# Performance work log

Hardware: AMD Instinct MI355X
Metric: run time of the kernel (lower is better)

Reference implementation:

```python
import jax, jax.numpy as jnp
import numpy as np

BS, T, N = 16, 48, 147
IN = 2 * N      # input_size = 294; lstm1 hidden = input_size
H = 128         # hidden_size
AH = 8          # transformer attention heads
GH = 4          # GAT heads
OUT = 294       # output_size
DFF = 2048      # TransformerEncoderLayer default dim_feedforward
NEG = -9e15

def _u(k, shape, fan):
    return jax.random.uniform(k, shape, jnp.float32, -1.0, 1.0) / np.sqrt(fan)

def setup_inputs():
    ks = iter(jax.random.split(jax.random.key(0), 40))
    p = {}
    p['X'] = jax.random.normal(next(ks), (BS, T, IN), jnp.float32)
    p['adj_matrix'] = jax.random.randint(next(ks), (N, N), 0, 2, jnp.int32)
    p['W_trans'] = _u(next(ks), (H, IN), IN); p['b_trans'] = jnp.zeros((H,), jnp.float32)
    p['enc_in_w'] = _u(next(ks), (3 * H, H), H); p['enc_in_b'] = jnp.zeros((3 * H,), jnp.float32)
    p['enc_out_w'] = _u(next(ks), (H, H), H); p['enc_out_b'] = jnp.zeros((H,), jnp.float32)
    p['ln1_g'] = jnp.ones((H,), jnp.float32); p['ln1_b'] = jnp.zeros((H,), jnp.float32)
    p['ln2_g'] = jnp.ones((H,), jnp.float32); p['ln2_b'] = jnp.zeros((H,), jnp.float32)
    p['ff1_w'] = _u(next(ks), (DFF, H), H); p['ff1_b'] = jnp.zeros((DFF,), jnp.float32)
    p['ff2_w'] = _u(next(ks), (H, DFF), DFF); p['ff2_b'] = jnp.zeros((H,), jnp.float32)
    p['Wih1'] = _u(next(ks), (4 * IN, H), H); p['Whh1'] = _u(next(ks), (4 * IN, IN), IN)
    p['bih1'] = jnp.zeros((4 * IN,), jnp.float32); p['bhh1'] = jnp.zeros((4 * IN,), jnp.float32)
    p['gat_W1'] = _u(next(ks), (GH, 2, H), 2); p['gat_a1'] = _u(next(ks), (GH, 2 * H), 2 * H)
    p['gat_W2'] = _u(next(ks), (GH * H, H), GH * H); p['gat_a2'] = _u(next(ks), (2 * H,), 2 * H)
    p['W_sc'] = _u(next(ks), (H, 2), 2); p['b_sc'] = jnp.zeros((H,), jnp.float32)
    p['Wih2'] = _u(next(ks), (4 * H, H * N), H * N); p['Whh2'] = _u(next(ks), (4 * H, H), H)
    p['bih2'] = jnp.zeros((4 * H,), jnp.float32); p['bhh2'] = jnp.zeros((4 * H,), jnp.float32)
    p['W_fc'] = _u(next(ks), (OUT, H), H); p['b_fc'] = jnp.zeros((OUT,), jnp.float32)
    return p

def _ln(x, g, b, eps=1e-5):
    m = x.mean(-1, keepdims=True)
    v = ((x - m) ** 2).mean(-1, keepdims=True)
    return (x - m) * jax.lax.rsqrt(v + eps) * g + b

def _mha(x, in_w, in_b, out_w, out_b):
    B, S, D = x.shape
    dh = D // AH
    q, k, v = jnp.split(x @ in_w.T + in_b, 3, axis=-1)
    def rh(t):
        return t.reshape(B, S, AH, dh).transpose(0, 2, 1, 3)
    q, k, v = rh(q), rh(k), rh(v)
    att = jax.nn.softmax(jnp.einsum('bhqd,bhkd->bhqk', q, k) / np.sqrt(dh), axis=-1)
    o = jnp.einsum('bhqk,bhkd->bhqd', att, v).transpose(0, 2, 1, 3).reshape(B, S, D)
    return o @ out_w.T + out_b

def _lstm(x, Wih, Whh, bih, bhh, hid):
    B = x.shape[0]
    def step(carry, xt):
        h, c = carry
        g = xt @ Wih.T + h @ Whh.T + (bih + bhh)
        i, f, gg, o = jnp.split(g, 4, axis=-1)
        c = jax.nn.sigmoid(f) * c + jax.nn.sigmoid(i) * jnp.tanh(gg)
        h = jax.nn.sigmoid(o) * jnp.tanh(c)
        return (h, c), h
    h0 = jnp.zeros((B, hid), x.dtype)
    (hT, _), ys = jax.lax.scan(step, (h0, h0), x.transpose(1, 0, 2))
    return ys.transpose(1, 0, 2), hT

def _gat(x, adj, W1, a1, W2, a2, alpha=0.1):
    # x: [B, N, 2]; batched over all bs*num_steps graph instances; eval mode (dropout off)
    mask = (adj > 0)[None, ...]
    # layer 1: GH heads, ELU + concat
    Wh = jnp.einsum('bnf,kfh->bknh', x, W1)                        # [B,GH,N,H]
    f1 = jnp.einsum('bknh,kh->bkn', Wh, a1[:, :H])
    f2 = jnp.einsum('bknh,kh->bkn', Wh, a1[:, H:])
    e = jax.nn.leaky_relu(f1[..., :, None] + f2[..., None, :], alpha)
    att = jax.nn.softmax(jnp.where(mask[:, None], e, NEG), axis=-1)
    h1 = jax.nn.elu(jnp.einsum('bkij,bkjh->bkih', att, Wh))        # [B,GH,N,H]
    h1 = h1.transpose(0, 2, 1, 3).reshape(x.shape[0], N, GH * H)   # concat heads
    # layer 2: single output head, final ELU
    Who = h1 @ W2                                                   # [B,N,H]
    g1 = Who @ a2[:H]
    g2 = Who @ a2[H:]
    e2 = jax.nn.leaky_relu(g1[..., :, None] + g2[..., None, :], alpha)
    att2 = jax.nn.softmax(jnp.where(mask, e2, NEG), axis=-1)
    return jax.nn.elu(jnp.einsum('bij,bjh->bih', att2, Who))        # [B,N,H]

def reference(X, adj_matrix, W_trans, b_trans, enc_in_w, enc_in_b, enc_out_w, enc_out_b,
              ln1_g, ln1_b, ln2_g, ln2_b, ff1_w, ff1_b, ff2_w, ff2_b,
              Wih1, Whh1, bih1, bhh1, gat_W1, gat_a1, gat_W2, gat_a2,
              W_sc, b_sc, Wih2, Whh2, bih2, bhh2, W_fc, b_fc):
    Y = jax.nn.elu(X @ W_trans.T + b_trans)                        # [BS,T,H]
    # TransformerEncoderLayer (post-norm, ReLU FFN, eval)
    Y = _ln(Y + _mha(Y, enc_in_w, enc_in_b, enc_out_w, enc_out_b), ln1_g, ln1_b)
    Y = _ln(Y + (jax.nn.relu(Y @ ff1_w.T + ff1_b) @ ff2_w.T + ff2_b), ln2_g, ln2_b)
    Y, _ = _lstm(Y, Wih1, Whh1, bih1, bhh1, IN)                    # [BS,T,2N]
    Yg = Y.reshape(N, BS * T, 2).transpose(1, 0, 2)                # raw reshape as in torch, -> [BS*T,N,2]
    out = _gat(Yg, adj_matrix, gat_W1, gat_a1, gat_W2, gat_a2)     # [BS*T,N,H]
    out = out.transpose(1, 0, 2).reshape(BS, T, N * H)             # stack(dim=1) then reshape
    sc = jax.nn.elu(X.reshape(BS, T, N, 2) @ W_sc.T + b_sc).reshape(BS, T, N * H)
    _, hT = _lstm(out + sc, Wih2, Whh2, bih2, bhh2, H)
    return hT @ W_fc.T + b_fc                                      # [BS,OUT]
```

## Files before the change

kernel.cpp:

```cpp
#include <hip/hip_runtime.h>
#include <math.h>


typedef _Float16 half8 __attribute__((ext_vector_type(8)));
typedef _Float16 half4 __attribute__((ext_vector_type(4)));
typedef _Float16 half2v __attribute__((ext_vector_type(2)));
typedef float f32x4 __attribute__((ext_vector_type(4)));

#if __has_builtin(__builtin_amdgcn_fdot2)
#define DOT2(a,b,c) __builtin_amdgcn_fdot2((a),(b),(c),false)
#else
#define DOT2(a,b,c) ((c) + (float)(a)[0]*(float)(b)[0] + (float)(a)[1]*(float)(b)[1])
#endif

static constexpr size_t Y0o   = 0;
static constexpr size_t QKVo  = 98304;
static constexpr size_t ATTOo = 393216;
static constexpr size_t Y1o   = 491520;
static constexpr size_t Y1Ho  = 589824;
static constexpr size_t FFHo  = 638976;
static constexpr size_t PREo  = 1425408;
static constexpr size_t Y2Ho  = 1523712;
static constexpr size_t XW1o  = 1572864;
static constexpr size_t Y3o   = 2476032;
static constexpr size_t Zo    = 0;
static constexpr size_t So    = 7225344;
static constexpr size_t WHOTo = 8354304;
static constexpr size_t WFo   = 16218624;
static constexpr size_t ZGPo  = 21035520;
static constexpr size_t ZGo   = 25754112;
static constexpr size_t HTo   = 26147328;
static constexpr size_t C12o  = 26149376;
static constexpr size_t WT1Ho = 26149392;
static constexpr size_t WT2Ho = 26323440;
static constexpr size_t FF1Ho = 26356208;
static constexpr size_t FF2Ho = 26487280;
static constexpr size_t WIH1Ho= 26618352;
static constexpr size_t W2To  = 26696176;
static constexpr size_t EINTo = 26728944;
static constexpr size_t EOUTTo= 26778096;
static constexpr size_t WTRTo = 26794480;
static constexpr size_t MASKo = 26832112;
static constexpr size_t HXo   = 26833008;

__device__ __forceinline__ float eluf(float x){ return x > 0.f ? x : __expf(x)-1.f; }
__device__ __forceinline__ float sigf(float x){ return 1.f/(1.f+__expf(-x)); }

__global__ void k_prep(const float* Whh1, const float* Whh2, const float* ff1w,
                       const float* ff2w, const float* Wih1, const float* einw,
                       const float* eoutw, const float* wtr, const float* gw2, float* ws) {
  int id = blockIdx.x * 256 + threadIdx.x;
  if (id < 348096) {
    int e=id&7, r=id>>3; int row=r%168; int q=r/168; int kg=q%37; int p=q/37;
    int k=kg*8+e; int gate=row/42, jr=row-gate*42; int j=gate*294+p*42+jr;
    ((_Float16*)(ws+WT1Ho))[id] = (_Float16)((k<294)? Whh1[j*294+k] : 0.f); return; }
  id -= 348096;
  if (id < 65536) {
    int e=id&7, r=id>>3; int j=r&511, gi=r>>9; int k=gi*8+e;
    ((_Float16*)(ws+WT2Ho))[id] = (_Float16)Whh2[j*128+k]; return; }
  id -= 65536;
  if (id < 262144) { ((_Float16*)(ws+FF1Ho))[id] = (_Float16)ff1w[id]; return; }
  id -= 262144;
  if (id < 262144) { ((_Float16*)(ws+FF2Ho))[id] = (_Float16)ff2w[id]; return; }
  id -= 262144;
  if (id < 155648) { int j=id>>7, k=id&127;
    ((_Float16*)(ws+WIH1Ho))[id] = (_Float16)((j<1176)? Wih1[j*128+k] : 0.f); return; }
  id -= 155648;
  if (id < 65536)  { int h=id>>9, q=id&511;
    ((_Float16*)(ws+W2To))[id] = (_Float16)gw2[q*128+h]; return; }
  id -= 65536;
  if (id < 49152)  { int k=id/384,  j=id-k*384;  ws[EINTo+id] = einw[j*128+k]; return; }
  id -= 49152;
  if (id < 16384)  { int k=id/128,  j=id-k*128;  ws[EOUTTo+id]= eoutw[j*128+k]; return; }
  id -= 16384;
  if (id < 37632)  { int k=id/128,  j=id-k*128;  ws[WTRTo+id] = wtr[j*294+k]; return; }
}

__global__ void k_c12_mask(const float* gw1, const float* ga1, const int* adj, float* ws) {
  int tid = threadIdx.x;
  if (tid < 8) {
    int k = tid>>1, c = tid&1;
    float a=0.f, b=0.f;
    for (int h=0; h<128; ++h) {
      float w = gw1[(k*2+c)*128+h];
      a += w * ga1[k*256+h];
      b += w * ga1[k*256+128+h];
    }
    ws[C12o+tid] = a; ws[C12o+8+tid] = b;
  }
  unsigned long long* msk = (unsigned long long*)(ws + MASKo);
  for (int i = tid; i < 441; i += 256) {
    int r = i/3, w = i-r*3;
    unsigned long long b = 0ull;
    for (int bit=0; bit<64; ++bit) {
      int j = w*64+bit;
      if (j < 147 && adj[r*147+j] > 0) b |= (1ull<<bit);
    }
    msk[i] = b;
  }
  unsigned* hx = (unsigned*)(ws + HXo);
  for (int i=tid;i<9408;i+=256) hx[i]=0u;
}

__global__ void k1_trans(const float* X, const float* btr, float* ws) {
  int row = blockIdx.x, tid = threadIdx.x;
  __shared__ float xr[294];
  for (int i=tid; i<294; i+=128) xr[i] = X[row*294+i];
  __syncthreads();
  float acc = btr[tid];
  const float* w = ws + WTRTo;
  for (int k=0;k<294;++k) acc += xr[k]*w[k*128+tid];
  ws[Y0o + (size_t)row*128 + tid] = eluf(acc);
}

__global__ void k2_qkv(const float* einb, float* ws) {
  int row = blockIdx.x, tid = threadIdx.x;
  __shared__ float yr[128];
  if (tid<128) yr[tid] = ws[Y0o+(size_t)row*128+tid];
  __syncthreads();
  float acc = einb[tid];
  const float* w = ws + EINTo;
  for (int k=0;k<128;++k) acc += yr[k]*w[k*384+tid];
  ws[QKVo + (size_t)row*384 + tid] = acc;
}

__global__ void k3_attn(float* ws) {
  int bid = blockIdx.x; int bs = bid>>3, a = bid&7; int tid = threadIdx.x;
  __shared__ float q[48][16], kk[48][16], v[48][16], sc[48][49];
  for (int idx=tid; idx<768; idx+=256) {
    int t = idx>>4, d = idx&15;
    const float* base = ws + QKVo + (size_t)(bs*48+t)*384 + a*16 + d;
    q[t][d] = base[0]; kk[t][d] = base[128]; v[t][d] = base[256];
  }
  __syncthreads();
  for (int idx=tid; idx<2304; idx+=256) {
    int i = idx/48, j = idx-i*48;
    float s = 0.f;
    for (int d=0;d<16;++d) s += q[i][d]*kk[j][d];
    sc[i][j] = s*0.25f;
  }
  __syncthreads();
  if (tid < 48) {
    float mx = -INFINITY;
    for (int j=0;j<48;++j) mx = fmaxf(mx, sc[tid][j]);
    float s = 0.f;
    for (int j=0;j<48;++j){ float p = __expf(sc[tid][j]-mx); sc[tid][j]=p; s+=p; }
    float inv = 1.f/s;
    for (int j=0;j<48;++j) sc[tid][j]*=inv;
  }
  __syncthreads();
  for (int idx=tid; idx<768; idx+=256) {
    int t = idx>>4, d = idx&15;
    float s=0.f;
    for (int j=0;j<48;++j) s += sc[t][j]*v[j][d];
    ws[ATTOo + (size_t)(bs*48+t)*128 + a*16 + d] = s;
  }
}

__global__ void k4_ln1(const float* eoutb, const float* g, const float* b, float* ws) {
  int row = blockIdx.x, tid = threadIdx.x;
  __shared__ float orow[128];
  __shared__ float red[128];
  __shared__ float mv[2];
  orow[tid] = ws[ATTOo+(size_t)row*128+tid];
  __syncthreads();
  float acc = eoutb[tid] + ws[Y0o+(size_t)row*128+tid];
  const float* w = ws + EOUTTo;
  for (int k=0;k<128;++k) acc += orow[k]*w[k*128+tid];
  red[tid]=acc; __syncthreads();
  for (int s=64;s>0;s>>=1){ if(tid<s) red[tid]+=red[tid+s]; __syncthreads(); }
  if (tid==0) mv[0]=red[0]*(1.f/128.f);
  __syncthreads();
  float d = acc - mv[0];
  red[tid]=d*d; __syncthreads();
  for (int s=64;s>0;s>>=1){ if(tid<s) red[tid]+=red[tid+s]; __syncthreads(); }
  if (tid==0) mv[1]=red[0]*(1.f/128.f);
  __syncthreads();
  float val = d*rsqrtf(mv[1]+1e-5f)*g[tid]+b[tid];
  ws[Y1o+(size_t)row*128+tid] = val;
  ((_Float16*)(ws+Y1Ho))[(size_t)row*128+tid] = (_Float16)val;
}

__global__ void __launch_bounds__(256) k5g(const float* b1, float* ws) {
  int tid=threadIdx.x; int gw=blockIdx.x*4+(tid>>6);
  int l=tid&63, lr=l&15, kg=l>>4;
  int mt=gw>>5, nt=gw&31;
  const _Float16* A=(const _Float16*)(ws+Y1Ho);
  const _Float16* B=(const _Float16*)(ws+FF1Ho);
  _Float16* C=(_Float16*)(ws+FFHo);
  size_t r0=(size_t)mt*64, c0=(size_t)nt*64;
  f32x4 acc[4][4];
  #pragma unroll
  for(int a=0;a<4;++a)
    #pragma unroll
    for(int b=0;b<4;++b) acc[a][b]=(f32x4){0.f,0.f,0.f,0.f};
  #pragma unroll
  for (int s=0;s<4;++s){
    int kb=s*32+kg*8;
    half8 av[4], bv[4];
    #pragma unroll
    for(int f=0;f<4;++f) av[f]=*(const half8*)(A+(r0+f*16+lr)*128+kb);
    #pragma unroll
    for(int f=0;f<4;++f) bv[f]=*(const half8*)(B+(c0+f*16+lr)*128+kb);
    #pragma unroll
    for(int fr=0;fr<4;++fr)
      #pragma unroll
      for(int fc=0;fc<4;++fc)
        acc[fr][fc]=__builtin_amdgcn_mfma_f32_16x16x32_f16(av[fr],bv[fc],acc[fr][fc],0,0,0);
  }
  #pragma unroll
  for(int fr=0;fr<4;++fr)
    #pragma unroll
    for(int fc=0;fc<4;++fc){
      size_t col=c0+fc*16+lr;
      float bb=b1[col];
      #pragma unroll
      for(int r=0;r<4;++r){
        float v=acc[fr][fc][r]+bb; v=fmaxf(v,0.f);
        C[(r0+fr*16+kg*4+r)*2048+col]=(_Float16)v;
      }
    }
}

__global__ void __launch_bounds__(256) k6g(float* ws) {
  int tid=threadIdx.x; int gw=blockIdx.x*4+(tid>>6);
  int l=tid&63, lr=l&15, kg=l>>4;
  int ksp=gw&3, nt=(gw>>2)&1, mt=gw>>3;
  const _Float16* A=(const _Float16*)(ws+FFHo);
  const _Float16* B=(const _Float16*)(ws+FF2Ho);
  float* C=ws+ZGPo+(size_t)ksp*98304;
  size_t r0=(size_t)mt*64, c0=(size_t)nt*64;
  f32x4 acc[4][4];
  #pragma unroll
  for(int a=0;a<4;++a)
    #pragma unroll
    for(int b=0;b<4;++b) acc[a][b]=(f32x4){0.f,0.f,0.f,0.f};
  #pragma unroll
  for (int s=0;s<16;++s){
    int kb=ksp*512+s*32+kg*8;
    half8 av[4], bv[4];
    #pragma unroll
    for(int f=0;f<4;++f) av[f]=*(const half8*)(A+(r0+f*16+lr)*2048+kb);
    #pragma unroll
    for(int f=0;f<4;++f) bv[f]=*(const half8*)(B+(c0+f*16+lr)*2048+kb);
    #pragma unroll
    for(int fr=0;fr<4;++fr)
      #pragma unroll
      for(int fc=0;fc<4;++fc)
        acc[fr][fc]=__builtin_amdgcn_mfma_f32_16x16x32_f16(av[fr],bv[fc],acc[fr][fc],0,0,0);
  }
  #pragma unroll
  for(int fr=0;fr<4;++fr)
    #pragma unroll
    for(int fc=0;fc<4;++fc){
      size_t col=c0+fc*16+lr;
      #pragma unroll
      for(int r=0;r<4;++r)
        C[(r0+fr*16+kg*4+r)*128+col]=acc[fr][fc][r];
    }
}

__global__ void k6b_ln2(const float* b2, const float* g, const float* b, float* ws) {
  int row=blockIdx.x, tid=threadIdx.x;
  __shared__ float red[128];
  __shared__ float mv[2];
  float acc = ws[Y1o+(size_t)row*128+tid] + b2[tid];
  #pragma unroll
  for (int ksp=0;ksp<4;++ksp) acc += ws[ZGPo+(size_t)ksp*98304+(size_t)row*128+tid];
  red[tid]=acc; __syncthreads();
  for (int s=64;s>0;s>>=1){ if(tid<s) red[tid]+=red[tid+s]; __syncthreads(); }
  if (tid==0) mv[0]=red[0]*(1.f/128.f);
  __syncthreads();
  float d = acc - mv[0];
  red[tid]=d*d; __syncthreads();
  for (int s=64;s>0;s>>=1){ if(tid<s) red[tid]+=red[tid+s]; __syncthreads(); }
  if (tid==0) mv[1]=red[0]*(1.f/128.f);
  __syncthreads();
  float val = d*rsqrtf(mv[1]+1e-5f)*g[tid]+b[tid];
  ((_Float16*)(ws+Y2Ho))[(size_t)row*128+tid] = (_Float16)val;
}

__global__ void __launch_bounds__(256) k7g(const float* bih1, const float* bhh1, float* ws) {
  int tid=threadIdx.x; int gw=blockIdx.x*4+(tid>>6);
  int l=tid&63, lr=l&15, kg=l>>4;
  int mt=gw/19, nt=gw-mt*19;
  const _Float16* A=(const _Float16*)(ws+Y2Ho);
  const _Float16* B=(const _Float16*)(ws+WIH1Ho);
  float* C=ws+XW1o;
  size_t r0=(size_t)mt*64, c0=(size_t)nt*64;
  f32x4 acc[4][4];
  #pragma unroll
  for(int a=0;a<4;++a)
    #pragma unroll
    for(int b=0;b<4;++b) acc[a][b]=(f32x4){0.f,0.f,0.f,0.f};
  #pragma unroll
  for (int s=0;s<4;++s){
    int kb=s*32+kg*8;
    half8 av[4], bv[4];
    #pragma unroll
    for(int f=0;f<4;++f) av[f]=*(const half8*)(A+(r0+f*16+lr)*128+kb);
    #pragma unroll
    for(int f=0;f<4;++f) bv[f]=*(const half8*)(B+(c0+f*16+lr)*128+kb);
    #pragma unroll
    for(int fr=0;fr<4;++fr)
      #pragma unroll
      for(int fc=0;fc<4;++fc)
        acc[fr][fc]=__builtin_amdgcn_mfma_f32_16x16x32_f16(av[fr],bv[fc],acc[fr][fc],0,0,0);
  }
  #pragma unroll
  for(int fr=0;fr<4;++fr)
    #pragma unroll
    for(int fc=0;fc<4;++fc){
      size_t col=c0+fc*16+lr;
      if (col<1176){
        float bb=bih1[col]+bhh1[col];
        #pragma unroll
        for(int r=0;r<4;++r)
          C[(r0+fr*16+kg*4+r)*1176+col]=acc[fr][fc][r]+bb;
      }
    }
}

__global__ void __launch_bounds__(256) k8_lstm1(float* ws) {
  int blk=blockIdx.x; int xcd=blk&7; int slot7=blk>>3;
  int b=xcd+8*(slot7/7), p=slot7%7; int tid=threadIdx.x;
  __shared__ __align__(16) _Float16 wl[49728];
  __shared__ __align__(16) _Float16 hls[296];
  __shared__ float gbuf[168];
  __shared__ float cloc[42];
  const half8* wsrc = (const half8*)((const _Float16*)(ws+WT1Ho) + (size_t)p*49728);
  for (int i=tid;i<6216;i+=256) ((half8*)wl)[i]=wsrc[i];
  if (tid<42) cloc[tid]=0.f;
  for (int i=tid;i<296;i+=256) hls[i]=(_Float16)0.f;
  unsigned* HX=(unsigned*)(ws+HXo);
  int gate=tid/42, jr=tid-gate*42;
  int j=(tid<168)? gate*294+p*42+jr : 0;
  float xw = (tid<168)? ws[XW1o+(size_t)(b*48)*1176+j] : 0.f;
  int own_lo=p*42;
  __syncthreads();
  for (int t=0;t<48;++t){
    if (tid<168){
      float a0=xw, a1=0.f;
      #pragma unroll
      for (int gi=0;gi<36;gi+=2){
        half8 w0=*(const half8*)&wl[((size_t)gi*168+tid)*8];
        half8 w1=*(const half8*)&wl[((size_t)(gi+1)*168+tid)*8];
        const half2v* h0=(const half2v*)&hls[gi*8];
        const half2v* h1=(const half2v*)&hls[(gi+1)*8];
        #pragma unroll
        for (int q=0;q<4;++q){
          half2v wp0={w0[2*q],w0[2*q+1]}; a0=DOT2(wp0,h0[q],a0);
          half2v wp1={w1[2*q],w1[2*q+1]}; a1=DOT2(wp1,h1[q],a1);
        }
      }
      {
        half8 w0=*(const half8*)&wl[((size_t)36*168+tid)*8];
        const half2v* h0=(const half2v*)&hls[36*8];
        #pragma unroll
        for (int q=0;q<4;++q){ half2v wp0={w0[2*q],w0[2*q+1]}; a0=DOT2(wp0,h0[q],a0); }
      }
      gbuf[tid]=a0+a1;
    }
    __syncthreads();
    if (tid<42){
      int k=p*42+tid;
      float ii=sigf(gbuf[tid]);
      float ff=sigf(gbuf[42+tid]);
      float gg=tanhf(gbuf[84+tid]);
      float oo=sigf(gbuf[126+tid]);
      float cn=ff*cloc[tid]+ii*gg; cloc[tid]=cn;
      float hn=oo*tanhf(cn);
      _Float16 hh=(_Float16)hn;
      hls[k]=hh;
      if (t<47){
        unsigned short pb; __builtin_memcpy(&pb,&hh,2);
        unsigned v=(((unsigned)(t+1))<<16)|(unsigned)pb;
        __hip_atomic_store(&HX[(unsigned)(((t+1)&1)*4704 + b*294 + k)], v,
                           __ATOMIC_RELAXED, __HIP_MEMORY_SCOPE_AGENT);
      }
      ws[Y3o+(size_t)(b*48+t)*294+k]=hn;
    }
    if (t<47){
      if (tid<168) xw = ws[XW1o+(size_t)(b*48+t+1)*1176+j];
      unsigned tag=(unsigned)(t+1);
      unsigned sb=(unsigned)(((t+1)&1)*4704 + b*294);
      if (tid>=42){
        int fi = tid-42;
        int u0 = (fi<own_lo)? fi : fi+42;
        unsigned v;
        for(;;){
          v=__hip_atomic_load(&HX[sb+u0],__ATOMIC_RELAXED,__HIP_MEMORY_SCOPE_AGENT);
          if ((v>>16)==tag) break;
          __builtin_amdgcn_s_sleep(1);
        }
        unsigned short pv=(unsigned short)(v&0xffffu);
        _Float16 hv; __builtin_memcpy(&hv,&pv,2);
        hls[u0]=hv;
        if (fi<38){
          int f1=fi+214;
          int u1=(f1<own_lo)? f1 : f1+42;
          for(;;){
            v=__hip_atomic_load(&HX[sb+u1],__ATOMIC_RELAXED,__HIP_MEMORY_SCOPE_AGENT);
            if ((v>>16)==tag) break;
            __builtin_amdgcn_s_sleep(1);
          }
          pv=(unsigned short)(v&0xffffu);
          __builtin_memcpy(&hv,&pv,2);
          hls[u1]=hv;
        }
      }
      __syncthreads();
    }
  }
}

__global__ void k10_gat1(float* ws) {
  int bid=blockIdx.x; int m=bid>>2, k=bid&3; int tid=threadIdx.x;
  __shared__ float x0[147],x1[147],f1[147],f2[147];
  __shared__ unsigned long long msk[441];
  for (int i=tid;i<294;i+=192){
    int n=i>>1,cc=i&1;
    float v=ws[Y3o + (size_t)n*1536 + m*2 + cc];
    if(cc==0)x0[n]=v; else x1[n]=v;
  }
  const unsigned long long* gm = (const unsigned long long*)(ws+MASKo);
  for (int i=tid;i<441;i+=192) msk[i]=gm[i];
  __syncthreads();
  float c10=ws[C12o+k*2], c11=ws[C12o+k*2+1], c20=ws[C12o+8+k*2], c21=ws[C12o+8+k*2+1];
  for (int i=tid;i<147;i+=192){ f1[i]=x0[i]*c10+x1[i]*c11; f2[i]=x0[i]*c20+x1[i]*c21; }
  __syncthreads();
  for (int i=tid;i<147;i+=192) {
    float fi=f1[i];
    float s=0.f,a0=0.f,a1=0.f;
    #pragma unroll
    for (int c=0;c<3;++c){
      unsigned long long mm=msk[i*3+c];
      int jn=(c<2)?64:19, jb=c*64;
      for (int jj=0;jj<jn;++jj){
        int jx=jb+jj;
        float e=fi+f2[jx];
        e=fmaxf(e,0.f)+0.1f*fminf(e,0.f);
        e=fminf(e,80.f);
        float pv=(mm&1ull)? __expf(e):0.f;
        s+=pv; a0+=pv*x0[jx]; a1+=pv*x1[jx];
        mm>>=1;
      }
    }
    float inv=1.f/s;
    size_t o = So + ((size_t)(m*4+k)*147+i)*2;
    ws[o]=a0*inv; ws[o+1]=a1*inv;
  }
}

__global__ void __launch_bounds__(256) k11_who(const float* gw1, float* ws) {
  int m=blockIdx.x, tid=threadIdx.x;
  int w=tid>>6, l=tid&63, lr=l&15, kg=l>>4;
  __shared__ float s0s[4][148], s1s[4][148];
  __shared__ float w1s[1024];
  __shared__ _Float16 h1t[160*72];
  for (int idx=tid; idx<588; idx+=256){
    int k=idx/147, i=idx-k*147;
    size_t o=So+((size_t)(m*4+k)*147+i)*2; s0s[k][i]=ws[o]; s1s[k][i]=ws[o+1];
  }
  for (int idx=tid; idx<1024; idx+=256) w1s[idx]=gw1[idx];
  f32x4 acc[10][2];
  #pragma unroll
  for(int a=0;a<10;++a){ acc[a][0]=(f32x4){0.f,0.f,0.f,0.f}; acc[a][1]=(f32x4){0.f,0.f,0.f,0.f}; }
  const _Float16* W2T = (const _Float16*)(ws+W2To);
  for (int q0=0;q0<512;q0+=64){
    __syncthreads();
    for (int idx=tid; idx<10240; idx+=256){
      int i=idx>>6, c=idx&63;
      _Float16 hv=(_Float16)0.f;
      if (i<147){
        int q=q0+c, k=q>>7, hp=q&127;
        float v=s0s[k][i]*w1s[k*256+hp]+s1s[k][i]*w1s[k*256+128+hp];
        hv=(_Float16)eluf(v);
      }
      h1t[i*72+c]=hv;
    }
    __syncthreads();
    #pragma unroll
    for (int ks2=0; ks2<2; ++ks2){
      int qq=q0+ks2*32;
      half8 bv0=*(const half8*)(W2T+(size_t)(w*32+lr)*512+qq+kg*8);
      half8 bv1=*(const half8*)(W2T+(size_t)(w*32+16+lr)*512+qq+kg*8);
      #pragma unroll
      for (int rf=0;rf<10;++rf){
        half8 av=*(const half8*)&h1t[(rf*16+lr)*72 + ks2*32 + kg*8];
        acc[rf][0]=__builtin_amdgcn_mfma_f32_16x16x32_f16(av,bv0,acc[rf][0],0,0,0);
        acc[rf][1]=__builtin_amdgcn_mfma_f32_16x16x32_f16(av,bv1,acc[rf][1],0,0,0);
      }
    }
  }
  _Float16* whoT=(_Float16*)(ws+WHOTo);
  #pragma unroll
  for (int rf=0;rf<10;++rf)
    #pragma unroll
    for (int cf=0;cf<2;++cf){
      int col=w*32+cf*16+lr;
      half4 hv = {(_Float16)acc[rf][cf][0],(_Float16)acc[rf][cf][1],
                  (_Float16)acc[rf][cf][2],(_Float16)acc[rf][cf][3]};
      *(half4*)&whoT[((size_t)m*128+col)*160 + rf*16+kg*4] = hv;
    }
}

__global__ void __launch_bounds__(256) k13_gat2(const float* X, const float* Wsc, const float* bsc,
                                               const float* ga2, float* ws) {
  int m=blockIdx.x, tid=threadIdx.x;
  int w=tid>>6, l=tid&63, lr=l&15, kg=l>>4;
  __shared__ _Float16 att_h[160*172];
  __shared__ float g1s[160], g2s[160];
  __shared__ float sre[160];
  __shared__ float a2s[256];
  __shared__ float wscs[256], bscs[128];
  __shared__ unsigned long long msk[441];
  _Float16* zf=(_Float16*)(ws+Zo);
  const _Float16* whoT=(const _Float16*)(ws+WHOTo);
  wscs[tid]=Wsc[tid];
  a2s[tid]=ga2[tid];
  if (tid<128) bscs[tid]=bsc[tid];
  const unsigned long long* gm=(const unsigned long long*)(ws+MASKo);
  for (int i=tid;i<441;i+=256) msk[i]=gm[i];
  __syncthreads();
  if (tid<160){
    float g1=0.f,g2=0.f;
    for (int h=0;h<128;++h){
      float v=(float)whoT[((size_t)m*128+h)*160+tid];
      g1+=v*a2s[h]; g2+=v*a2s[128+h];
    }
    g1s[tid]=g1; g2s[tid]=g2;
  }
  __syncthreads();
  if (tid<160){
    if (tid<147){
      float gi=g1s[tid];
      float s=0.f;
      #pragma unroll
      for (int c=0;c<3;++c){
        unsigned long long mm=msk[tid*3+c];
        int jn=(c<2)?64:19, jb=c*64;
        for (int jj=0;jj<jn;++jj){
          float e=gi+g2s[jb+jj];
          e=fmaxf(e,0.f)+0.1f*fminf(e,0.f);
          e=fminf(e,11.f);
          float pv=(mm&1ull)? __expf(e):0.f;
          att_h[tid*172+jb+jj]=(_Float16)pv;
          s+=pv;
          mm>>=1;
        }
      }
      sre[tid]=1.f/s;
      for (int jx=147;jx<160;++jx) att_h[tid*172+jx]=(_Float16)0.f;
    } else {
      sre[tid]=0.f;
      for (int jx=0;jx<160;++jx) att_h[tid*172+jx]=(_Float16)0.f;
    }
  }
  __syncthreads();
  f32x4 acc[10][2];
  #pragma unroll
  for (int a=0;a<10;++a){ acc[a][0]=(f32x4){0.f,0.f,0.f,0.f}; acc[a][1]=(f32x4){0.f,0.f,0.f,0.f}; }
  int c0=w*32+lr, c1=w*32+16+lr;
  #pragma unroll
  for (int s=0;s<5;++s){
    int j0=s*32;
    half8 bv0=*(const half8*)&whoT[((size_t)m*128+c0)*160+j0+kg*8];
    half8 bv1=*(const half8*)&whoT[((size_t)m*128+c1)*160+j0+kg*8];
    #pragma unroll
    for (int rf=0;rf<10;++rf){
      half8 av=*(const half8*)&att_h[(rf*16+lr)*172+j0+kg*8];
      acc[rf][0]=__builtin_amdgcn_mfma_f32_16x16x32_f16(av,bv0,acc[rf][0],0,0,0);
      acc[rf][1]=__builtin_amdgcn_mfma_f32_16x16x32_f16(av,bv1,acc[rf][1],0,0,0);
    }
  }
  #pragma unroll
  for (int rf=0;rf<10;++rf)
    #pragma unroll
    for (int r_=0;r_<4;++r_){
      int row=rf*16+kg*4+r_;
      if (row<147){
        float inv=sre[row];
        int gbase=row*98304+m*128;
        int bs=gbase/903168; int r2=gbase-bs*903168;
        int t=r2/18816; int qb=r2-t*18816;
        int nn=qb>>7;
        const float* xr=X+(size_t)(bs*48+t)*294+nn*2;
        float x0=xr[0],x1=xr[1];
        size_t zb=(size_t)(bs*48+t)*18816+qb;
        #pragma unroll
        for (int cf=0;cf<2;++cf){
          int col=w*32+cf*16+lr;
          float pv=acc[rf][cf][r_]*inv;
          float sv=x0*wscs[col*2]+x1*wscs[col*2+1]+bscs[col];
          zf[zb+col]=(_Float16)(eluf(pv)+eluf(sv));
        }
      }
    }
}

__global__ void kWconv(const float* Wih2, float* ws) {
  size_t i = ((size_t)blockIdx.x*256 + threadIdx.x)*4;
  _Float16* wf = (_Float16*)(ws + WFo);
  float4 v = *(const float4*)&Wih2[i];
  half4 h = {(_Float16)v.x, (_Float16)v.y, (_Float16)v.z, (_Float16)v.w};
  *(half4*)&wf[i] = h;
}

__global__ void __launch_bounds__(512) k14_tile(float* ws) {
  int tid=threadIdx.x;
  int wave=tid>>6, l=tid&63, lr=l&15, kg=l>>4;
  int wm=wave>>2, wn=wave&3;
  int m0=blockIdx.x*256, n0=blockIdx.y*256, ks=blockIdx.z;
  const _Float16* A=(const _Float16*)(ws+Zo);
  const _Float16* B=(const _Float16*)(ws+WFo);
  __shared__ _Float16 As[2][256*40];
  __shared__ _Float16 Bs[2][256*40];
  f32x4 acc[8][4];
  #pragma unroll
  for (int a=0;a<8;++a)
    #pragma unroll
    for (int b=0;b<4;++b) acc[a][b]=(f32x4){0.f,0.f,0.f,0.f};
  int kbase=ks*1568;
  int row=tid>>2, seg=tid&3;
  {
    int kb=kbase;
    *(half8*)&As[0][(size_t)row*40+seg*8]       = *(const half8*)(A+(size_t)(m0+row)*18816+kb+seg*8);
    *(half8*)&As[0][(size_t)(row+128)*40+seg*8] = *(const half8*)(A+(size_t)(m0+row+128)*18816+kb+seg*8);
    *(half8*)&Bs[0][(size_t)row*40+seg*8]       = *(const half8*)(B+(size_t)(n0+row)*18816+kb+seg*8);
    *(half8*)&Bs[0][(size_t)(row+128)*40+seg*8] = *(const half8*)(B+(size_t)(n0+row+128)*18816+kb+seg*8);
  }
  __syncthreads();
  for (int c=0;c<49;++c){
    int cur=c&1, nxt=cur^1;
    if (c<48){
      int kb=kbase+(c+1)*32;
      *(half8*)&As[nxt][(size_t)row*40+seg*8]       = *(const half8*)(A+(size_t)(m0+row)*18816+kb+seg*8);
      *(half8*)&As[nxt][(size_t)(row+128)*40+seg*8] = *(const half8*)(A+(size_t)(m0+row+128)*18816+kb+seg*8);
      *(half8*)&Bs[nxt][(size_t)row*40+seg*8]       = *(const half8*)(B+(size_t)(n0+row)*18816+kb+seg*8);
      *(half8*)&Bs[nxt][(size_t)(row+128)*40+seg*8] = *(const half8*)(B+(size_t)(n0+row+128)*18816+kb+seg*8);
    }
    half8 bfr[4], afr[8];
    #pragma unroll
    for (int fn=0;fn<4;++fn) bfr[fn]=*(const half8*)&Bs[cur][(size_t)(wn*64+fn*16+lr)*40+kg*8];
    #pragma unroll
    for (int fm=0;fm<8;++fm) afr[fm]=*(const half8*)&As[cur][(size_t)(wm*128+fm*16+lr)*40+kg*8];
    #pragma unroll
    for (int fm=0;fm<8;++fm)
      #pragma unroll
      for (int fn=0;fn<4;++fn)
        acc[fm][fn]=__builtin_amdgcn_mfma_f32_16x16x32_f16(afr[fm],bfr[fn],acc[fm][fn],0,0,0);
    __syncthreads();
  }
  float* P = ws + ZGPo + (size_t)ks*393216;
  #pragma unroll
  for (int fm=0;fm<8;++fm)
    #pragma unroll
    for (int fn=0;fn<4;++fn)
      #pragma unroll
      for (int r=0;r<4;++r)
        P[(size_t)(m0+wm*128+fm*16+kg*4+r)*512 + n0+wn*64+fn*16+lr] = acc[fm][fn][r];
}

__global__ void k14b_red(const float* bih2, const float* bhh2, float* ws) {
  int i = blockIdx.x*256+threadIdx.x;
  int g = i & 511;
  float s = bih2[g]+bhh2[g];
  #pragma unroll
  for (int ks=0;ks<12;++ks) s += ws[ZGPo + (size_t)ks*393216 + i];
  ws[ZGo + i] = s;
}

__global__ void __launch_bounds__(512) k15_lstm2(float* ws) {
  int b=blockIdx.x, tid=threadIdx.x;
  __shared__ __align__(16) _Float16 wl[65536];
  __shared__ __align__(16) _Float16 hs[128];
  __shared__ float cc[128], g[512];
  const half8* wsrc=(const half8*)(ws+WT2Ho);
  for (int i=tid;i<8192;i+=512) ((half8*)wl)[i]=wsrc[i];
  if (tid<128){hs[tid]=(_Float16)0.f; cc[tid]=0.f;}
  __syncthreads();
  for (int t=0;t<48;++t){
    int row=b*48+t;
    float a0=ws[ZGo+(size_t)row*512+tid], a1=0.f;
    #pragma unroll
    for (int gi=0;gi<16;gi+=2){
      half8 w0=*(const half8*)&wl[((size_t)gi*512+tid)*8];
      half8 w1=*(const half8*)&wl[((size_t)(gi+1)*512+tid)*8];
      const half2v* h0=(const half2v*)&hs[gi*8];
      const half2v* h1=(const half2v*)&hs[(gi+1)*8];
      #pragma unroll
      for (int q=0;q<4;++q){
        half2v wp0={w0[2*q],w0[2*q+1]}; a0=DOT2(wp0,h0[q],a0);
        half2v wp1={w1[2*q],w1[2*q+1]}; a1=DOT2(wp1,h1[q],a1);
      }
    }
    g[tid]=a0+a1;
    __syncthreads();
    if (tid<128){
      float ii=sigf(g[tid]);
      float ff=sigf(g[128+tid]);
      float gg=tanhf(g[256+tid]);
      float oo=sigf(g[384+tid]);
      float cn=ff*cc[tid]+ii*gg; cc[tid]=cn;
      float hn=oo*tanhf(cn);
      hs[tid]=(_Float16)hn;
      if (t==47) ws[HTo+b*128+tid]=hn;
    }
    __syncthreads();
  }
}

__global__ void k16_fc(const float* Wfc, const float* bfc, float* out, float* ws) {
  int b=blockIdx.x, tid=threadIdx.x;
  __shared__ float hr[128];
  if (tid<128) hr[tid]=ws[HTo+b*128+tid];
  __syncthreads();
  if (tid<294){
    float acc=bfc[tid];
    const float* wr=Wfc+tid*128;
    for (int k=0;k<128;++k) acc+=hr[k]*wr[k];
    out[b*294+tid]=acc;
  }
}

extern "C" void kernel_launch(void* const* d_in, const int* in_sizes, int n_in,
                              void* d_out, int out_size, void* d_ws, size_t ws_size,
                              hipStream_t stream) {
  const float* X    =(const float*)d_in[0];
  const int*   adj  =(const int*)  d_in[1];
  const float* Wtr  =(const float*)d_in[2];
  const float* btr  =(const float*)d_in[3];
  const float* einw =(const float*)d_in[4];
  const float* einb =(const float*)d_in[5];
  const float* eoutw=(const float*)d_in[6];
  const float* eoutb=(const float*)d_in[7];
  const float* ln1g =(const float*)d_in[8];
  const float* ln1b =(const float*)d_in[9];
  const float* ln2g =(const float*)d_in[10];
  const float* ln2b =(const float*)d_in[11];
  const float* ff1w =(const float*)d_in[12];
  const float* ff1b =(const float*)d_in[13];
  const float* ff2w =(const float*)d_in[14];
  const float* ff2b =(const float*)d_in[15];
  const float* Wih1 =(const float*)d_in[16];
  const float* Whh1 =(const float*)d_in[17];
  const float* bih1 =(const float*)d_in[18];
  const float* bhh1 =(const float*)d_in[19];
  const float* gw1  =(const float*)d_in[20];
  const float* ga1  =(const float*)d_in[21];
  const float* gw2  =(const float*)d_in[22];
  const float* ga2  =(const float*)d_in[23];
  const float* Wsc  =(const float*)d_in[24];
  const float* bsc  =(const float*)d_in[25];
  const float* Wih2 =(const float*)d_in[26];
  const float* Whh2 =(const float*)d_in[27];
  const float* bih2 =(const float*)d_in[28];
  const float* bhh2 =(const float*)d_in[29];
  const float* Wfc  =(const float*)d_in[30];
  const float* bfc  =(const float*)d_in[31];
  float* ws=(float*)d_ws;
  float* out=(float*)d_out;

  k_prep<<<dim3(4931),dim3(256),0,stream>>>(Whh1,Whh2,ff1w,ff2w,Wih1,einw,eoutw,Wtr,gw2,ws);
  k_c12_mask<<<dim3(1),dim3(256),0,stream>>>(gw1,ga1,adj,ws);
  k1_trans<<<dim3(768),dim3(128),0,stream>>>(X,btr,ws);
  k2_qkv<<<dim3(768),dim3(384),0,stream>>>(einb,ws);
  k3_attn<<<dim3(128),dim3(256),0,stream>>>(ws);
  k4_ln1<<<dim3(768),dim3(128),0,stream>>>(eoutb,ln1g,ln1b,ws);
  k5g<<<dim3(96),dim3(256),0,stream>>>(ff1b,ws);
  k6g<<<dim3(24),dim3(256),0,stream>>>(ws);
  k6b_ln2<<<dim3(768),dim3(128),0,stream>>>(ff2b,ln2g,ln2b,ws);
  k7g<<<dim3(57),dim3(256),0,stream>>>(bih1,bhh1,ws);
  k8_lstm1<<<dim3(112),dim3(256),0,stream>>>(ws);
  k10_gat1<<<dim3(3072),dim3(192),0,stream>>>(ws);
  k11_who<<<dim3(768),dim3(256),0,stream>>>(gw1,ws);
  k13_gat2<<<dim3(768),dim3(256),0,stream>>>(X,Wsc,bsc,ga2,ws);
  kWconv<<<dim3(9408),dim3(256),0,stream>>>(Wih2,ws);
  k14_tile<<<dim3(3,2,12),dim3(512),0,stream>>>(ws);
  k14b_red<<<dim3(1536),dim3(256),0,stream>>>(bih2,bhh2,ws);
  k15_lstm2<<<dim3(16),dim3(512),0,stream>>>(ws);
  k16_fc<<<dim3(16),dim3(320),0,stream>>>(Wfc,bfc,out,ws);
}
```

Measured before the change: 501.6 us.

## Fuse GAT who-projection into attention kernel and merge trans with QKV

Merges the GAT output-projection kernel with the second GAT attention kernel so the per-graph transformed features stay in shared memory instead of round-tripping through global workspace. Also fuses the input transform with the QKV projection into a single launch. This removes a large intermediate global write/read and two kernel launches, at the cost of much larger LDS usage per block (lower occupancy) and idle threads during the transform phase.

```diff
diff --git a/kernel.cpp b/kernel.cpp
--- a/kernel.cpp
+++ b/kernel.cpp
@@ -19,13 +19,11 @@
 static constexpr size_t Y1o   = 491520;
 static constexpr size_t Y1Ho  = 589824;
 static constexpr size_t FFHo  = 638976;
-static constexpr size_t PREo  = 1425408;
 static constexpr size_t Y2Ho  = 1523712;
 static constexpr size_t XW1o  = 1572864;
 static constexpr size_t Y3o   = 2476032;
 static constexpr size_t Zo    = 0;
 static constexpr size_t So    = 7225344;
-static constexpr size_t WHOTo = 8354304;
 static constexpr size_t WFo   = 16218624;
 static constexpr size_t ZGPo  = 21035520;
 static constexpr size_t ZGo   = 25754112;
@@ -102,21 +100,20 @@
   for (int i=tid;i<9408;i+=256) hx[i]=0u;
 }
 
-__global__ void k1_trans(const float* X, const float* btr, float* ws) {
+__global__ void k1_qkv(const float* X, const float* btr, const float* einb, float* ws) {
   int row = blockIdx.x, tid = threadIdx.x;
   __shared__ float xr[294];
-  for (int i=tid; i<294; i+=128) xr[i] = X[row*294+i];
-  __syncthreads();
-  float acc = btr[tid];
-  const float* w = ws + WTRTo;
-  for (int k=0;k<294;++k) acc += xr[k]*w[k*128+tid];
-  ws[Y0o + (size_t)row*128 + tid] = eluf(acc);
-}
-
-__global__ void k2_qkv(const float* einb, float* ws) {
-  int row = blockIdx.x, tid = threadIdx.x;
   __shared__ float yr[128];
-  if (tid<128) yr[tid] = ws[Y0o+(size_t)row*128+tid];
+  for (int i=tid; i<294; i+=384) xr[i] = X[row*294+i];
+  __syncthreads();
+  if (tid<128){
+    float acc = btr[tid];
+    const float* w = ws + WTRTo;
+    for (int k=0;k<294;++k) acc += xr[k]*w[k*128+tid];
+    float v = eluf(acc);
+    yr[tid]=v;
+    ws[Y0o + (size_t)row*128 + tid] = v;
+  }
   __syncthreads();
   float acc = einb[tid];
   const float* w = ws + EINTo;
@@ -452,81 +449,77 @@
   }
 }
 
-__global__ void __launch_bounds__(256) k11_who(const float* gw1, float* ws) {
+__global__ void __launch_bounds__(256) k12_gat(const float* gw1, const float* ga2,
+                                              const float* X, const float* Wsc, const float* bsc,
+                                              float* ws) {
   int m=blockIdx.x, tid=threadIdx.x;
   int w=tid>>6, l=tid&63, lr=l&15, kg=l>>4;
   __shared__ float s0s[4][148], s1s[4][148];
   __shared__ float w1s[1024];
   __shared__ _Float16 h1t[160*72];
+  __shared__ _Float16 whoL[128*168];
+  __shared__ _Float16 att_h[160*172];
+  __shared__ float g1s[160], g2s[160], sre[160];
+  __shared__ float a2s[256], wscs[256], bscs[128];
+  __shared__ unsigned long long msk[441];
+  _Float16* zf=(_Float16*)(ws+Zo);
   for (int idx=tid; idx<588; idx+=256){
     int k=idx/147, i=idx-k*147;
     size_t o=So+((size_t)(m*4+k)*147+i)*2; s0s[k][i]=ws[o]; s1s[k][i]=ws[o+1];
   }
   for (int idx=tid; idx<1024; idx+=256) w1s[idx]=gw1[idx];
-  f32x4 acc[10][2];
-  #pragma unroll
-  for(int a=0;a<10;++a){ acc[a][0]=(f32x4){0.f,0.f,0.f,0.f}; acc[a][1]=(f32x4){0.f,0.f,0.f,0.f}; }
-  const _Float16* W2T = (const _Float16*)(ws+W2To);
-  for (int q0=0;q0<512;q0+=64){
-    __syncthreads();
-    for (int idx=tid; idx<10240; idx+=256){
-      int i=idx>>6, c=idx&63;
-      _Float16 hv=(_Float16)0.f;
-      if (i<147){
-        int q=q0+c, k=q>>7, hp=q&127;
-        float v=s0s[k][i]*w1s[k*256+hp]+s1s[k][i]*w1s[k*256+128+hp];
-        hv=(_Float16)eluf(v);
-      }
-      h1t[i*72+c]=hv;
-    }
-    __syncthreads();
-    #pragma unroll
-    for (int ks2=0; ks2<2; ++ks2){
-      int qq=q0+ks2*32;
-      half8 bv0=*(const half8*)(W2T+(size_t)(w*32+lr)*512+qq+kg*8);
-      half8 bv1=*(const half8*)(W2T+(size_t)(w*32+16+lr)*512+qq+kg*8);
-      #pragma unroll
-      for (int rf=0;rf<10;++rf){
-        half8 av=*(const half8*)&h1t[(rf*16+lr)*72 + ks2*32 + kg*8];
-        acc[rf][0]=__builtin_amdgcn_mfma_f32_16x16x32_f16(av,bv0,acc[rf][0],0,0,0);
-        acc[rf][1]=__builtin_amdgcn_mfma_f32_16x16x32_f16(av,bv1,acc[rf][1],0,0,0);
-      }
-    }
-  }
-  _Float16* whoT=(_Float16*)(ws+WHOTo);
-  #pragma unroll
-  for (int rf=0;rf<10;++rf)
-    #pragma unroll
-    for (int cf=0;cf<2;++cf){
-      int col=w*32+cf*16+lr;
-      half4 hv = {(_Float16)acc[rf][cf][0],(_Float16)acc[rf][cf][1],
-                  (_Float16)acc[rf][cf][2],(_Float16)acc[rf][cf][3]};
-      *(half4*)&whoT[((size_t)m*128+col)*160 + rf*16+kg*4] = hv;
-    }
-}
-
-__global__ void __launch_bounds__(256) k13_gat2(const float* X, const float* Wsc, const float* bsc,
-                                               const float* ga2, float* ws) {
-  int m=blockIdx.x, tid=threadIdx.x;
-  int w=tid>>6, l=tid&63, lr=l&15, kg=l>>4;
-  __shared__ _Float16 att_h[160*172];
-  __shared__ float g1s[160], g2s[160];
-  __shared__ float sre[160];
-  __shared__ float a2s[256];
-  __shared__ float wscs[256], bscs[128];
-  __shared__ unsigned long long msk[441];
-  _Float16* zf=(_Float16*)(ws+Zo);
-  const _Float16* whoT=(const _Float16*)(ws+WHOTo);
+  a2s[tid]=ga2[tid];
   wscs[tid]=Wsc[tid];
-  a2s[tid]=ga2[tid];
   if (tid<128) bscs[tid]=bsc[tid];
   const unsigned long long* gm=(const unsigned long long*)(ws+MASKo);
   for (int i=tid;i<441;i+=256) msk[i]=gm[i];
+  {
+    f32x4 acc[10][2];
+    #pragma unroll
+    for(int a=0;a<10;++a){ acc[a][0]=(f32x4){0.f,0.f,0.f,0.f}; acc[a][1]=(f32x4){0.f,0.f,0.f,0.f}; }
+    const _Float16* W2T = (const _Float16*)(ws+W2To);
+    for (int q0=0;q0<512;q0+=64){
+      __syncthreads();
+      for (int idx=tid; idx<10240; idx+=256){
+        int i=idx>>6, c=idx&63;
+        _Float16 hv=(_Float16)0.f;
+        if (i<147){
+          int q=q0+c, k=q>>7, hp=q&127;
+          float v=s0s[k][i]*w1s[k*256+hp]+s1s[k][i]*w1s[k*256+128+hp];
+          hv=(_Float16)eluf(v);
+        }
+        h1t[i*72+c]=hv;
+      }
+      __syncthreads();
+      #pragma unroll
+      for (int ks2=0; ks2<2; ++ks2){
+        int qq=q0+ks2*32;
+        half8 bv0=*(const half8*)(W2T+(size_t)(w*32+lr)*512+qq+kg*8);
+        half8 bv1=*(const half8*)(W2T+(size_t)(w*32+16+lr)*512+qq+kg*8);
+        #pragma unroll
+        for (int rf=0;rf<10;++rf){
+          half8 av=*(const half8*)&h1t[(rf*16+lr)*72 + ks2*32 + kg*8];
+          acc[rf][0]=__builtin_amdgcn_mfma_f32_16x16x32_f16(av,bv0,acc[rf][0],0,0,0);
+          acc[rf][1]=__builtin_amdgcn_mfma_f32_16x16x32_f16(av,bv1,acc[rf][1],0,0,0);
+        }
+      }
+    }
+    __syncthreads();
+    #pragma unroll
+    for (int rf=0;rf<10;++rf)
+      #pragma unroll
+      for (int cf=0;cf<2;++cf){
+        int col=w*32+cf*16+lr;
+        half4 hv = {(_Float16)acc[rf][cf][0],(_Float16)acc[rf][cf][1],
+                    (_Float16)acc[rf][cf][2],(_Float16)acc[rf][cf][3]};
+        *(half4*)&whoL[col*168 + rf*16+kg*4] = hv;
+      }
+  }
   __syncthreads();
   if (tid<160){
     float g1=0.f,g2=0.f;
     for (int h=0;h<128;++h){
-      float v=(float)whoT[((size_t)m*128+h)*160+tid];
+      float v=(float)whoL[h*168+tid];
       g1+=v*a2s[h]; g2+=v*a2s[128+h];
     }
     g1s[tid]=g1; g2s[tid]=g2;
@@ -565,8 +558,8 @@
   #pragma unroll
   for (int s=0;s<5;++s){
     int j0=s*32;
-    half8 bv0=*(const half8*)&whoT[((size_t)m*128+c0)*160+j0+kg*8];
-    half8 bv1=*(const half8*)&whoT[((size_t)m*128+c1)*160+j0+kg*8];
+    half8 bv0=*(const half8*)&whoL[c0*168+j0+kg*8];
+    half8 bv1=*(const half8*)&whoL[c1*168+j0+kg*8];
     #pragma unroll
     for (int rf=0;rf<10;++rf){
       half8 av=*(const half8*)&att_h[(rf*16+lr)*172+j0+kg*8];
@@ -764,8 +757,7 @@
 
   k_prep<<<dim3(4931),dim3(256),0,stream>>>(Whh1,Whh2,ff1w,ff2w,Wih1,einw,eoutw,Wtr,gw2,ws);
   k_c12_mask<<<dim3(1),dim3(256),0,stream>>>(gw1,ga1,adj,ws);
-  k1_trans<<<dim3(768),dim3(128),0,stream>>>(X,btr,ws);
-  k2_qkv<<<dim3(768),dim3(384),0,stream>>>(einb,ws);
+  k1_qkv<<<dim3(768),dim3(384),0,stream>>>(X,btr,einb,ws);
   k3_attn<<<dim3(128),dim3(256),0,stream>>>(ws);
   k4_ln1<<<dim3(768),dim3(128),0,stream>>>(eoutb,ln1g,ln1b,ws);
   k5g<<<dim3(96),dim3(256),0,stream>>>(ff1b,ws);
@@ -774,8 +766,7 @@
   k7g<<<dim3(57),dim3(256),0,stream>>>(bih1,bhh1,ws);
   k8_lstm1<<<dim3(112),dim3(256),0,stream>>>(ws);
   k10_gat1<<<dim3(3072),dim3(192),0,stream>>>(ws);
-  k11_who<<<dim3(768),dim3(256),0,stream>>>(gw1,ws);
-  k13_gat2<<<dim3(768),dim3(256),0,stream>>>(X,Wsc,bsc,ga2,ws);
+  k12_gat<<<dim3(768),dim3(256),0,stream>>>(gw1,ga2,X,Wsc,bsc,ws);
   kWconv<<<dim3(9408),dim3(256),0,stream>>>(Wih2,ws);
   k14_tile<<<dim3(3,2,12),dim3(512),0,stream>>>(ws);
   k14b_red<<<dim3(1536),dim3(256),0,stream>>>(bih2,bhh2,ws);
```

Measured after the change: 574.3 us. 1.14x slower.
